# Performance work log

Hardware: AMD Instinct MI355X
Metric: run time of the kernel (lower is better)

The kernel has to match this reference:

```python
import jax, jax.numpy as jnp
import numpy as np

DIM = 1024
HEADS = 16
HIDDEN = 4 * DIM


def layernorm(x, g, b, eps=1e-5):
    mu = jnp.mean(x, axis=-1, keepdims=True)
    var = jnp.mean(jnp.square(x - mu), axis=-1, keepdims=True)
    return (x - mu) * jax.lax.rsqrt(var + eps) * g + b


def setup_inputs() -> dict:
    key = jax.random.key(0)
    ks = jax.random.split(key, 8)
    s = DIM ** -0.5
    return {
        "x": jax.random.normal(ks[0], (2, 2048, DIM), dtype=jnp.float32),
        "ln1_g": jnp.ones((DIM,), jnp.float32),
        "ln1_b": jnp.zeros((DIM,), jnp.float32),
        "qkv_w": jax.random.normal(ks[1], (DIM, 3 * DIM), jnp.float32) * s,
        "proj_w": jax.random.normal(ks[2], (DIM, DIM), jnp.float32) * s,
        "proj_b": jnp.zeros((DIM,), jnp.float32),
        "ln2_g": jnp.ones((DIM,), jnp.float32),
        "ln2_b": jnp.zeros((DIM,), jnp.float32),
        "fc1_w": jax.random.normal(ks[3], (DIM, HIDDEN), jnp.float32) * s,
        "fc1_b": jnp.zeros((HIDDEN,), jnp.float32),
        "fc2_w": jax.random.normal(ks[4], (HIDDEN, DIM), jnp.float32) * (HIDDEN ** -0.5),
        "fc2_b": jnp.zeros((DIM,), jnp.float32),
    }


def block_fwd(x, ln1_g, ln1_b, qkv_w, proj_w, proj_b, ln2_g, ln2_b,
              fc1_w, fc1_b, fc2_w, fc2_b):
    B, N, C = x.shape
    H = HEADS
    Dh = C // H
    scale = Dh ** -0.5
    # --- attention branch (pre-norm) ---
    h = layernorm(x, ln1_g, ln1_b)
    qkv = h @ qkv_w                     # [B,N,3C] (no bias: qkv_bias=False)
    qkv = qkv.reshape(B, N, 3, H, Dh)
    q = qkv[:, :, 0].transpose(0, 2, 1, 3)   # [B,H,N,Dh]
    k = qkv[:, :, 1].transpose(0, 2, 1, 3)
    v = qkv[:, :, 2].transpose(0, 2, 1, 3)
    attn = jnp.einsum('bhqd,bhkd->bhqk', q, k) * scale
    attn = jax.nn.softmax(attn, axis=-1)
    o = jnp.einsum('bhqk,bhkd->bhqd', attn, v)
    o = o.transpose(0, 2, 1, 3).reshape(B, N, C)
    x = x + (o @ proj_w + proj_b)
    # --- MLP branch (pre-norm) ---
    h = layernorm(x, ln2_g, ln2_b)
    h = jax.nn.gelu(h @ fc1_w + fc1_b, approximate=False)  # torch nn.GELU = exact erf
    x = x + (h @ fc2_w + fc2_b)
    return x


def reference(x, ln1_g, ln1_b, qkv_w, proj_w, proj_b, ln2_g, ln2_b,
              fc1_w, fc1_b, fc2_w, fc2_b):
    return block_fwd(x, ln1_g, ln1_b, qkv_w, proj_w, proj_b, ln2_g, ln2_b,
                     fc1_w, fc1_b, fc2_w, fc2_b)
```

## Files before the change

kernel.cpp:

```cpp
#include <hip/hip_runtime.h>
#include <math.h>

typedef unsigned short u16;
typedef unsigned int u32;
typedef __attribute__((ext_vector_type(8))) short short8;
typedef __attribute__((ext_vector_type(4))) float f32x4;
typedef __attribute__((ext_vector_type(2))) u32 u32x2;
typedef __attribute__((ext_vector_type(4))) u32 u32x4;
typedef __attribute__((ext_vector_type(4))) u16 u16x4;

typedef __attribute__((address_space(1))) const void gmem_t;
typedef __attribute__((address_space(3))) void lmem_t;

__device__ __forceinline__ u16 f2bf(float f) {
  u32 u = __builtin_bit_cast(u32, f);
  u = u + 0x7fffu + ((u >> 16) & 1u);
  return (u16)(u >> 16);
}

__device__ __forceinline__ u32 cvt_pk_bf16(float a, float b) {
  u32 r;
  asm("v_cvt_pk_bf16_f32 %0, %1, %2" : "=v"(r) : "v"(a), "v"(b));
  return r;
}

__device__ __forceinline__ void g2l16(const void* g, void* l) {
  __builtin_amdgcn_global_load_lds((gmem_t*)g, (lmem_t*)l, 16, 0, 0);
}

__global__ __launch_bounds__(256) void wtrans(const float* __restrict__ in,
                                              u16* __restrict__ out, int R, int C) {
  __shared__ float t[64][65];
  int tid = threadIdx.x;
  int nbx = C >> 6;
  int bx = blockIdx.x % nbx, by = blockIdx.x / nbx;
  int r0 = by << 6, c0 = bx << 6;
  int lr = tid >> 2, lc = (tid & 3) << 4;
  const float* src = in + (size_t)(r0 + lr) * C + c0 + lc;
#pragma unroll
  for (int j = 0; j < 4; ++j) {
    f32x4 v = *(const f32x4*)(src + j * 4);
    t[lr][lc + j * 4 + 0] = v.x; t[lr][lc + j * 4 + 1] = v.y;
    t[lr][lc + j * 4 + 2] = v.z; t[lr][lc + j * 4 + 3] = v.w;
  }
  __syncthreads();
  int oc = tid >> 2, orr = (tid & 3) << 4;
  u16* dst = out + (size_t)(c0 + oc) * R + r0 + orr;
  u32 u[8];
#pragma unroll
  for (int j = 0; j < 8; ++j)
    u[j] = (u32)f2bf(t[orr + 2 * j][oc]) | ((u32)f2bf(t[orr + 2 * j + 1][oc]) << 16);
  u32x4 v0; v0.x = u[0]; v0.y = u[1]; v0.z = u[2]; v0.w = u[3];
  u32x4 v1; v1.x = u[4]; v1.y = u[5]; v1.z = u[6]; v1.w = u[7];
  *(u32x4*)(dst) = v0;
  *(u32x4*)(dst + 8) = v1;
}

__global__ __launch_bounds__(256) void lnorm(const float* __restrict__ in,
                                             const float* __restrict__ gw,
                                             const float* __restrict__ bw,
                                             u16* __restrict__ out) {
  int r = blockIdx.x, tid = threadIdx.x;
  const f32x4 v = *((const f32x4*)(in + (size_t)r * 1024) + tid);
  float s = v.x + v.y + v.z + v.w;
  float ss = v.x * v.x + v.y * v.y + v.z * v.z + v.w * v.w;
#pragma unroll
  for (int o = 32; o >= 1; o >>= 1) { s += __shfl_xor(s, o); ss += __shfl_xor(ss, o); }
  __shared__ float red[8];
  int w = tid >> 6;
  if ((tid & 63) == 0) { red[w] = s; red[4 + w] = ss; }
  __syncthreads();
  s = red[0] + red[1] + red[2] + red[3];
  ss = red[4] + red[5] + red[6] + red[7];
  float mu = s * (1.0f / 1024.0f);
  float var = ss * (1.0f / 1024.0f) - mu * mu;
  float rstd = rsqrtf(var + 1e-5f);
  const f32x4 g4 = *((const f32x4*)gw + tid);
  const f32x4 b4 = *((const f32x4*)bw + tid);
  u16x4 o;
  o.x = f2bf((v.x - mu) * rstd * g4.x + b4.x);
  o.y = f2bf((v.y - mu) * rstd * g4.y + b4.y);
  o.z = f2bf((v.z - mu) * rstd * g4.z + b4.z);
  o.w = f2bf((v.w - mu) * rstd * g4.w + b4.w);
  *((u16x4*)(out + (size_t)r * 1024) + tid) = o;
}

template <int EPI, int BM, int BN>
__global__ __launch_bounds__(256) void gemm_bt(
    const u16* __restrict__ A, const u16* __restrict__ BT, int M, int N, int K,
    const float* __restrict__ bias, const float* __restrict__ resid,
    float* __restrict__ fout, u16* __restrict__ bout,
    u16* __restrict__ bout2, u16* __restrict__ bout3) {
  constexpr int AIT = BM / 64, BIT = BN / 64;
  constexpr int MR = BM / 32, NR = BN / 32;
  __shared__ __align__(16) u16 smA[BM * 32];
  __shared__ __align__(16) u16 smB[BN * 32];
  int tid = threadIdx.x;
  int w = tid >> 6, l = tid & 63, lq = l & 15, g = l >> 4;
  int nbx = N / BN;
  int t = (int)blockIdx.x;
  int cpx = (int)gridDim.x >> 3;
  t = (t & 7) * cpx + (t >> 3);
  int by = t / nbx, bx = t - by * nbx;
  long brow = (long)by * BM, bcol = (long)bx * BN;
  int wr = w >> 1, wc = w & 1;

  const u16* aS[AIT]; const u16* bS[BIT];
#pragma unroll
  for (int it = 0; it < AIT; ++it) {
    int p = it * 256 + tid;
    int row = p >> 2;
    int gc = (p & 3) ^ (row & 3);
    aS[it] = A + (size_t)(brow + row) * K + gc * 8;
  }
#pragma unroll
  for (int it = 0; it < BIT; ++it) {
    int p = it * 256 + tid;
    int row = p >> 2;
    int gc = (p & 3) ^ (row & 3);
    bS[it] = BT + (size_t)(bcol + row) * K + gc * 8;
  }
  f32x4 zero = {0.f, 0.f, 0.f, 0.f};
  f32x4 acc[MR][NR];
#pragma unroll
  for (int m = 0; m < MR; ++m)
#pragma unroll
    for (int n = 0; n < NR; ++n) acc[m][n] = zero;

  for (int k0 = 0; k0 < K; k0 += 32) {
#pragma unroll
    for (int it = 0; it < AIT; ++it) g2l16(aS[it] + k0, &smA[it * 2048 + w * 512]);
#pragma unroll
    for (int it = 0; it < BIT; ++it) g2l16(bS[it] + k0, &smB[it * 2048 + w * 512]);
    __syncthreads();
    short8 af[MR], bfb[NR];
#pragma unroll
    for (int m = 0; m < MR; ++m) {
      int r = wr * (BM / 2) + m * 16 + lq;
      af[m] = *(const short8*)((const char*)smA + (r * 64 + ((g * 16) ^ ((r & 3) << 4))));
    }
#pragma unroll
    for (int n = 0; n < NR; ++n) {
      int r = wc * (BN / 2) + n * 16 + lq;
      bfb[n] = *(const short8*)((const char*)smB + (r * 64 + ((g * 16) ^ ((r & 3) << 4))));
    }
#pragma unroll
    for (int m = 0; m < MR; ++m)
#pragma unroll
      for (int n = 0; n < NR; ++n)
        acc[m][n] = __builtin_amdgcn_mfma_f32_16x16x32_bf16(af[m], bfb[n], acc[m][n], 0, 0, 0);
    __syncthreads();
  }

  long colbase = bcol + wc * (BN / 2);
#pragma unroll
  for (int m = 0; m < MR; ++m) {
#pragma unroll
    for (int n = 0; n < NR; ++n) {
      f32x4 v = acc[m][n];
      long col = colbase + n * 16 + lq;
      long row0 = brow + wr * (BM / 2) + m * 16 + g * 4;
      if constexpr (EPI == 0) {
        int part = (int)(bcol >> 10);
        long colq = col - ((long)part << 10);
        int hh = (int)(colq >> 6), d = (int)(colq & 63);
#pragma unroll
        for (int i = 0; i < 4; ++i) {
          long row = row0 + i;
          long b = row >> 11, nq = row & 2047;
          long bh = b * 16 + hh;
          u16 val = f2bf(v[i]);
          if (part == 0)      bout [(bh * 2048 + nq) * 64 + d] = val;
          else if (part == 1) bout2[(bh * 2048 + nq) * 64 + d] = val;
          else                bout3[(bh * 64 + d) * 2048 + nq] = val;
        }
      } else if constexpr (EPI == 1 || EPI == 3) {
        float bb = bias[col];
#pragma unroll
        for (int i = 0; i < 4; ++i) {
          long idx = (row0 + i) * N + col;
          fout[idx] = resid[idx] + v[i] + bb;
        }
      } else {
        float bb = bias[col];
#pragma unroll
        for (int i = 0; i < 4; ++i) {
          float xg = v[i] + bb;
          float ge = 0.5f * xg * (1.0f + erff(xg * 0.70710678118654752f));
          bout[(row0 + i) * N + col] = f2bf(ge);
        }
      }
    }
  }
}

__global__ __launch_bounds__(256, 2) void attn_fwd(const u16* __restrict__ qb,
                                                   const u16* __restrict__ kb,
                                                   const u16* __restrict__ vtb,
                                                   u16* __restrict__ ob) {
  __shared__ __align__(16) u16 kl[2][64 * 64];
  __shared__ __align__(16) u16 vl[2][64 * 64];
  __shared__ __align__(16) u16 pl[4][32 * 72];
  int tid = threadIdx.x;
  int w = tid >> 6, l = tid & 63, lq = l & 15, g = l >> 4;
  int bh = (int)blockIdx.x & 31;
  int qt = (int)blockIdx.x >> 5;

  const u16* qr = qb + ((size_t)bh * 2048 + qt * 128 + w * 32 + lq) * 64 + g * 8;
  short8 qA0 = *(const short8*)qr;
  short8 qA1 = *(const short8*)(qr + 32);
  short8 qB0 = *(const short8*)(qr + 16 * 64);
  short8 qB1 = *(const short8*)(qr + 16 * 64 + 32);

  const u16* kS[2]; const u16* vS[2];
#pragma unroll
  for (int it = 0; it < 2; ++it) {
    int p = it * 256 + tid;
    int row = p >> 3;
    int gc = (p & 7) ^ (row & 7);
    kS[it] = kb + ((size_t)bh * 2048 + row) * 64 + gc * 8;
    vS[it] = vtb + ((size_t)bh * 64 + row) * 2048 + gc * 8;
  }
  auto issue = [&](int buf, int kt0) {
#pragma unroll
    for (int it = 0; it < 2; ++it) {
      g2l16(kS[it] + (size_t)kt0 * 64, &kl[buf][it * 2048 + w * 512]);
      g2l16(vS[it] + kt0,              &vl[buf][it * 2048 + w * 512]);
    }
  };

  f32x4 zero = {0.f, 0.f, 0.f, 0.f};
  f32x4 accO0[4] = {zero, zero, zero, zero};
  f32x4 accO1[4] = {zero, zero, zero, zero};
  f32x4 accl0 = zero, accl1 = zero;
  const float sc = 0.125f * 1.44269504088896f;
  u32x4 ov; ov.x = ov.y = ov.z = ov.w = 0x3F803F80u;
  short8 onesf = __builtin_bit_cast(short8, ov);

  issue(0, 0);
  for (int t = 0; t < 32; ++t) {
    int cur = t & 1;
    issue(cur ^ 1, ((t + 1) & 31) << 6);
    asm volatile("s_waitcnt vmcnt(4)" ::: "memory");
    __builtin_amdgcn_s_barrier();
    asm volatile("" ::: "memory");

    const char* klc = (const char*)&kl[cur][0];
    const char* vlc = (const char*)&vl[cur][0];

    f32x4 s0[4], s1[4];
#pragma unroll
    for (int kt = 0; kt < 4; ++kt) {
      int r = kt * 16 + lq;
      short8 a0 = *(const short8*)(klc + (r * 128 + ((g * 16) ^ ((r & 7) << 4))));
      short8 a1 = *(const short8*)(klc + (r * 128 + ((g * 16 + 64) ^ ((r & 7) << 4))));
      s0[kt] = __builtin_amdgcn_mfma_f32_16x16x32_bf16(a0, qA0, zero, 0, 0, 0);
      s0[kt] = __builtin_amdgcn_mfma_f32_16x16x32_bf16(a1, qA1, s0[kt], 0, 0, 0);
      s1[kt] = __builtin_amdgcn_mfma_f32_16x16x32_bf16(a0, qB0, zero, 0, 0, 0);
      s1[kt] = __builtin_amdgcn_mfma_f32_16x16x32_bf16(a1, qB1, s1[kt], 0, 0, 0);
    }

    char* plw = (char*)&pl[w][0];
#pragma unroll
    for (int kt = 0; kt < 4; ++kt) {
      u32x2 uA, uB;
      uA.x = cvt_pk_bf16(exp2f(s0[kt][0] * sc - 12.0f), exp2f(s0[kt][1] * sc - 12.0f));
      uA.y = cvt_pk_bf16(exp2f(s0[kt][2] * sc - 12.0f), exp2f(s0[kt][3] * sc - 12.0f));
      uB.x = cvt_pk_bf16(exp2f(s1[kt][0] * sc - 12.0f), exp2f(s1[kt][1] * sc - 12.0f));
      uB.y = cvt_pk_bf16(exp2f(s1[kt][2] * sc - 12.0f), exp2f(s1[kt][3] * sc - 12.0f));
      *(u32x2*)(plw + lq * 144 + kt * 32 + g * 8) = uA;
      *(u32x2*)(plw + 2304 + lq * 144 + kt * 32 + g * 8) = uB;
    }

#pragma unroll
    for (int c = 0; c < 2; ++c) {
      short8 paA = *(const short8*)(plw + lq * 144 + g * 16 + c * 64);
      short8 paB = *(const short8*)(plw + 2304 + lq * 144 + g * 16 + c * 64);
#pragma unroll
      for (int dt = 0; dt < 4; ++dt) {
        int r = dt * 16 + lq;
        short8 b = *(const short8*)(vlc + (r * 128 + ((g * 16 + c * 64) ^ ((r & 7) << 4))));
        accO0[dt] = __builtin_amdgcn_mfma_f32_16x16x32_bf16(paA, b, accO0[dt], 0, 0, 0);
        accO1[dt] = __builtin_amdgcn_mfma_f32_16x16x32_bf16(paB, b, accO1[dt], 0, 0, 0);
      }
      accl0 = __builtin_amdgcn_mfma_f32_16x16x32_bf16(paA, onesf, accl0, 0, 0, 0);
      accl1 = __builtin_amdgcn_mfma_f32_16x16x32_bf16(paB, onesf, accl1, 0, 0, 0);
    }
    asm volatile("" ::: "memory");
    __builtin_amdgcn_s_barrier();
  }

  float li0[4], li1[4];
#pragma unroll
  for (int i = 0; i < 4; ++i) { li0[i] = 1.0f / accl0[i]; li1[i] = 1.0f / accl1[i]; }
  int b = bh >> 4, h = bh & 15;
  long qbase = (long)qt * 128 + w * 32 + g * 4;
#pragma unroll
  for (int dt = 0; dt < 4; ++dt)
#pragma unroll
    for (int i = 0; i < 4; ++i) {
      long d = dt * 16 + lq;
      ob[((long)b * 2048 + qbase + i) * 1024 + h * 64 + d]      = f2bf(accO0[dt][i] * li0[i]);
      ob[((long)b * 2048 + qbase + 16 + i) * 1024 + h * 64 + d] = f2bf(accO1[dt][i] * li1[i]);
    }
}

extern "C" void kernel_launch(void* const* d_in, const int* in_sizes, int n_in,
                              void* d_out, int out_size, void* d_ws, size_t ws_size,
                              hipStream_t stream) {
  const float* x     = (const float*)d_in[0];
  const float* ln1g  = (const float*)d_in[1];
  const float* ln1b  = (const float*)d_in[2];
  const float* qkvw  = (const float*)d_in[3];
  const float* projw = (const float*)d_in[4];
  const float* projb = (const float*)d_in[5];
  const float* ln2g  = (const float*)d_in[6];
  const float* ln2b  = (const float*)d_in[7];
  const float* fc1w  = (const float*)d_in[8];
  const float* fc1b  = (const float*)d_in[9];
  const float* fc2w  = (const float*)d_in[10];
  const float* fc2b  = (const float*)d_in[11];
  char* ws = (char*)d_ws;
  u16* qkv_wt  = (u16*)(ws + 0);
  u16* proj_wt = (u16*)(ws + 6291456);
  u16* fc1_wt  = (u16*)(ws + 8388608);
  u16* fc2_wt  = (u16*)(ws + 16777216);
  u16* h       = (u16*)(ws + 25165824);
  u16* qbuf    = (u16*)(ws + 33554432);
  u16* kbuf    = (u16*)(ws + 41943040);
  u16* vtbuf   = (u16*)(ws + 50331648);
  u16* aout    = (u16*)(ws + 58720256);
  float* y1    = (float*)(ws + 67108864);
  u16* gbuf    = (u16*)(ws + 33554432);
  float* outp  = (float*)d_out;

  wtrans<<<768, 256, 0, stream>>>(qkvw, qkv_wt, 1024, 3072);
  wtrans<<<256, 256, 0, stream>>>(projw, proj_wt, 1024, 1024);
  wtrans<<<1024, 256, 0, stream>>>(fc1w, fc1_wt, 1024, 4096);
  wtrans<<<1024, 256, 0, stream>>>(fc2w, fc2_wt, 4096, 1024);

  lnorm<<<4096, 256, 0, stream>>>(x, ln1g, ln1b, h);
  gemm_bt<0, 128, 128><<<768, 256, 0, stream>>>(h, qkv_wt, 4096, 3072, 1024,
                                      nullptr, nullptr, nullptr, qbuf, kbuf, vtbuf);
  attn_fwd<<<512, 256, 0, stream>>>(qbuf, kbuf, vtbuf, aout);
  gemm_bt<1, 64, 128><<<512, 256, 0, stream>>>(aout, proj_wt, 4096, 1024, 1024,
                                      projb, x, y1, nullptr, nullptr, nullptr);
  lnorm<<<4096, 256, 0, stream>>>(y1, ln2g, ln2b, h);
  gemm_bt<2, 128, 128><<<1024, 256, 0, stream>>>(h, fc1_wt, 4096, 4096, 1024,
                                       fc1b, nullptr, nullptr, gbuf, nullptr, nullptr);
  gemm_bt<3, 64, 128><<<512, 256, 0, stream>>>(gbuf, fc2_wt, 4096, 1024, 4096,
                                      fc2b, y1, outp, nullptr, nullptr, nullptr);
}
```

Measured before the change: 303.0 us.

## Double-buffer GEMM LDS tiles with BK=64 and async prefetch

Reworks the bf16 GEMM main loop to use two LDS buffers with 64-wide K tiles, issuing the next tile's global-to-LDS loads before computing on the current one. A vmcnt wait replaces the full __syncthreads, and the swizzle is widened to 8 chunks. The aim is to hide global load latency and halve the barrier count per K. In exchange, LDS use grows fourfold per block, which can lower occupancy, so launch bounds now request 2 blocks per CU.

```diff
diff --git a/kernel.cpp b/kernel.cpp
--- a/kernel.cpp
+++ b/kernel.cpp
@@ -26,6 +26,14 @@
 
 __device__ __forceinline__ void g2l16(const void* g, void* l) {
   __builtin_amdgcn_global_load_lds((gmem_t*)g, (lmem_t*)l, 16, 0, 0);
+}
+
+template <int N> __device__ __forceinline__ void waitcnt_vm() {
+  if constexpr (N == 0)      asm volatile("s_waitcnt vmcnt(0)" ::: "memory");
+  else if constexpr (N == 4) asm volatile("s_waitcnt vmcnt(4)" ::: "memory");
+  else if constexpr (N == 6) asm volatile("s_waitcnt vmcnt(6)" ::: "memory");
+  else if constexpr (N == 8) asm volatile("s_waitcnt vmcnt(8)" ::: "memory");
+  else static_assert(N == 0 || N == 4 || N == 6 || N == 8, "add literal");
 }
 
 __global__ __launch_bounds__(256) void wtrans(const float* __restrict__ in,
@@ -86,15 +94,16 @@
 }
 
 template <int EPI, int BM, int BN>
-__global__ __launch_bounds__(256) void gemm_bt(
+__global__ __launch_bounds__(256, 2) void gemm_bt(
     const u16* __restrict__ A, const u16* __restrict__ BT, int M, int N, int K,
     const float* __restrict__ bias, const float* __restrict__ resid,
     float* __restrict__ fout, u16* __restrict__ bout,
     u16* __restrict__ bout2, u16* __restrict__ bout3) {
-  constexpr int AIT = BM / 64, BIT = BN / 64;
+  constexpr int AIT = BM / 32, BIT = BN / 32;
+  constexpr int L = AIT + BIT;
   constexpr int MR = BM / 32, NR = BN / 32;
-  __shared__ __align__(16) u16 smA[BM * 32];
-  __shared__ __align__(16) u16 smB[BN * 32];
+  __shared__ __align__(16) u16 smA[2][BM * 64];
+  __shared__ __align__(16) u16 smB[2][BN * 64];
   int tid = threadIdx.x;
   int w = tid >> 6, l = tid & 63, lq = l & 15, g = l >> 4;
   int nbx = N / BN;
@@ -109,17 +118,24 @@
 #pragma unroll
   for (int it = 0; it < AIT; ++it) {
     int p = it * 256 + tid;
-    int row = p >> 2;
-    int gc = (p & 3) ^ (row & 3);
+    int row = p >> 3;
+    int gc = (p & 7) ^ (row & 7);
     aS[it] = A + (size_t)(brow + row) * K + gc * 8;
   }
 #pragma unroll
   for (int it = 0; it < BIT; ++it) {
     int p = it * 256 + tid;
-    int row = p >> 2;
-    int gc = (p & 3) ^ (row & 3);
+    int row = p >> 3;
+    int gc = (p & 7) ^ (row & 7);
     bS[it] = BT + (size_t)(bcol + row) * K + gc * 8;
   }
+  auto STAGE = [&](int buf, int k0) {
+#pragma unroll
+    for (int it = 0; it < AIT; ++it) g2l16(aS[it] + k0, &smA[buf][it * 2048 + w * 512]);
+#pragma unroll
+    for (int it = 0; it < BIT; ++it) g2l16(bS[it] + k0, &smB[buf][it * 2048 + w * 512]);
+  };
+
   f32x4 zero = {0.f, 0.f, 0.f, 0.f};
   f32x4 acc[MR][NR];
 #pragma unroll
@@ -127,30 +143,41 @@
 #pragma unroll
     for (int n = 0; n < NR; ++n) acc[m][n] = zero;
 
-  for (int k0 = 0; k0 < K; k0 += 32) {
-#pragma unroll
-    for (int it = 0; it < AIT; ++it) g2l16(aS[it] + k0, &smA[it * 2048 + w * 512]);
-#pragma unroll
-    for (int it = 0; it < BIT; ++it) g2l16(bS[it] + k0, &smB[it * 2048 + w * 512]);
-    __syncthreads();
-    short8 af[MR], bfb[NR];
-#pragma unroll
-    for (int m = 0; m < MR; ++m) {
-      int r = wr * (BM / 2) + m * 16 + lq;
-      af[m] = *(const short8*)((const char*)smA + (r * 64 + ((g * 16) ^ ((r & 3) << 4))));
-    }
-#pragma unroll
-    for (int n = 0; n < NR; ++n) {
-      int r = wc * (BN / 2) + n * 16 + lq;
-      bfb[n] = *(const short8*)((const char*)smB + (r * 64 + ((g * 16) ^ ((r & 3) << 4))));
-    }
-#pragma unroll
-    for (int m = 0; m < MR; ++m)
-#pragma unroll
-      for (int n = 0; n < NR; ++n)
-        acc[m][n] = __builtin_amdgcn_mfma_f32_16x16x32_bf16(af[m], bfb[n], acc[m][n], 0, 0, 0);
-    __syncthreads();
-  }
+  int NT = K >> 6;
+  STAGE(0, 0);
+  for (int tt = 0; tt < NT; ++tt) {
+    int cur = tt & 1;
+    int knext = ((tt + 1) == NT ? 0 : (tt + 1)) << 6;
+    STAGE(cur ^ 1, knext);
+    waitcnt_vm<L>();
+    __builtin_amdgcn_s_barrier();
+    asm volatile("" ::: "memory");
+
+    const char* sA = (const char*)&smA[cur][0];
+    const char* sB = (const char*)&smB[cur][0];
+#pragma unroll
+    for (int c = 0; c < 2; ++c) {
+      short8 af[MR], bfb[NR];
+#pragma unroll
+      for (int m = 0; m < MR; ++m) {
+        int r = wr * (BM / 2) + m * 16 + lq;
+        af[m] = *(const short8*)(sA + r * 128 + ((g * 16 + c * 64) ^ ((r & 7) << 4)));
+      }
+#pragma unroll
+      for (int n = 0; n < NR; ++n) {
+        int r = wc * (BN / 2) + n * 16 + lq;
+        bfb[n] = *(const short8*)(sB + r * 128 + ((g * 16 + c * 64) ^ ((r & 7) << 4)));
+      }
+#pragma unroll
+      for (int m = 0; m < MR; ++m)
+#pragma unroll
+        for (int n = 0; n < NR; ++n)
+          acc[m][n] = __builtin_amdgcn_mfma_f32_16x16x32_bf16(af[m], bfb[n], acc[m][n], 0, 0, 0);
+    }
+    asm volatile("" ::: "memory");
+    __builtin_amdgcn_s_barrier();
+  }
+  waitcnt_vm<0>();
 
   long colbase = bcol + wc * (BN / 2);
 #pragma unroll
@@ -241,7 +268,7 @@
   for (int t = 0; t < 32; ++t) {
     int cur = t & 1;
     issue(cur ^ 1, ((t + 1) & 31) << 6);
-    asm volatile("s_waitcnt vmcnt(4)" ::: "memory");
+    waitcnt_vm<4>();
     __builtin_amdgcn_s_barrier();
     asm volatile("" ::: "memory");
 
@@ -289,6 +316,7 @@
     asm volatile("" ::: "memory");
     __builtin_amdgcn_s_barrier();
   }
+  waitcnt_vm<0>();
 
   float li0[4], li1[4];
 #pragma unroll
```

After: 280.2 us. -7.5%, faster.
